# Performance work log

Measured on AMD Instinct MI355X. Metric: run time of the kernel, lower is better.

Reference implementation:

```python
import jax, jax.numpy as jnp
import numpy as np

N_HOST, N_FLOW = 20000, 200000
D_HOST, D_FLOW, D_H, D_OUT, L = 64, 128, 256, 2, 2
E = 2000000


def _mean_agg(x_src, src, dst, num_dst):
    # SAGEConv default 'mean' neighbor aggregation: mean of source features per destination node.
    msg = x_src[src]                                            # [E, D]
    s = jax.ops.segment_sum(msg, dst, num_segments=num_dst)     # [num_dst, D]
    cnt = jax.ops.segment_sum(jnp.ones((src.shape[0],), x_src.dtype), dst, num_segments=num_dst)
    return s / jnp.maximum(cnt, 1.0)[:, None]


def setup_inputs() -> dict:
    key = jax.random.key(0)
    ks = jax.random.split(key, 20)
    s = 0.02
    inp = {
        'x_host': jax.random.normal(ks[0], (N_HOST, D_HOST), jnp.float32),
        'x_flow': jax.random.normal(ks[1], (N_FLOW, D_FLOW), jnp.float32),
        'eidx_hf_src': jax.random.randint(ks[2], (E,), 0, N_HOST, jnp.int32),
        'eidx_hf_dst': jax.random.randint(ks[3], (E,), 0, N_FLOW, jnp.int32),
        'eidx_fh_src': jax.random.randint(ks[4], (E,), 0, N_FLOW, jnp.int32),
        'eidx_fh_dst': jax.random.randint(ks[5], (E,), 0, N_HOST, jnp.int32),
        'host_proj_W': jax.random.normal(ks[6], (D_HOST, D_H), jnp.float32) * s,
        'host_proj_b': jnp.zeros((D_H,), jnp.float32),
        'flow_proj_W': jax.random.normal(ks[7], (D_FLOW, D_H), jnp.float32) * s,
        'flow_proj_b': jnp.zeros((D_H,), jnp.float32),
        # per-layer SAGEConv params: lin_l (neighbor agg, with bias), lin_r (root, no bias)
        'Wl_hf': jax.random.normal(ks[8], (L, D_H, D_H), jnp.float32) * s,
        'bl_hf': jnp.zeros((L, D_H), jnp.float32),
        'Wr_hf': jax.random.normal(ks[9], (L, D_H, D_H), jnp.float32) * s,
        'Wl_fh': jax.random.normal(ks[10], (L, D_H, D_H), jnp.float32) * s,
        'bl_fh': jnp.zeros((L, D_H), jnp.float32),
        'Wr_fh': jax.random.normal(ks[11], (L, D_H, D_H), jnp.float32) * s,
        'lin_W': jax.random.normal(ks[12], (D_H, D_OUT), jnp.float32) * s,
        'lin_b': jnp.zeros((D_OUT,), jnp.float32),
    }
    return inp


def reference(x_host, x_flow, eidx_hf_src, eidx_hf_dst, eidx_fh_src, eidx_fh_dst,
              host_proj_W, host_proj_b, flow_proj_W, flow_proj_b,
              Wl_hf, bl_hf, Wr_hf, Wl_fh, bl_fh, Wr_fh, lin_W, lin_b):
    n_host, n_flow = x_host.shape[0], x_flow.shape[0]
    h = jax.nn.relu(x_host @ host_proj_W + host_proj_b)   # [n_host, D_H]
    f = jax.nn.relu(x_flow @ flow_proj_W + flow_proj_b)   # [n_flow, D_H]
    for i in range(Wl_hf.shape[0]):
        # host -> flow SAGEConv
        agg_f = _mean_agg(h, eidx_hf_src, eidx_hf_dst, n_flow)
        new_f = agg_f @ Wl_hf[i] + bl_hf[i] + f @ Wr_hf[i]
        # flow -> host SAGEConv
        agg_h = _mean_agg(f, eidx_fh_src, eidx_fh_dst, n_host)
        new_h = agg_h @ Wl_fh[i] + bl_fh[i] + h @ Wr_fh[i]
        h = jax.nn.leaky_relu(new_h, 0.01)
        f = jax.nn.leaky_relu(new_f, 0.01)
    return f @ lin_W + lin_b  # logits for flow nodes [n_flow, D_OUT]
```

## Files before the change

### kernel.cpp

```cpp
#include <hip/hip_runtime.h>

#define NH    20000
#define NF    200000
#define DHOST 64
#define DFLOW 128
#define DHID  256
#define NE    2000000

typedef __attribute__((ext_vector_type(8))) short s16x8;
typedef __attribute__((ext_vector_type(4))) float f32x4;

__device__ __forceinline__ unsigned short f2bf(float x) {
    unsigned u = __builtin_bit_cast(unsigned, x);
    unsigned r = (u + 0x7fffu + ((u >> 16) & 1u)) >> 16;
    return (unsigned short)r;
}
__device__ __forceinline__ float bf2f(unsigned short h) {
    unsigned u = ((unsigned)h) << 16;
    return __builtin_bit_cast(float, u);
}

typedef const __attribute__((address_space(1))) unsigned int guint;
typedef __attribute__((address_space(3))) unsigned int luint;
__device__ __forceinline__ void gld16(const void* g, void* l) {
    __builtin_amdgcn_global_load_lds((guint*)g, (luint*)l, 16, 0, 0);
}

__device__ __forceinline__ void dq8(uint2 u, float s, float* a) {
#pragma unroll
    for (int j = 0; j < 4; ++j) {
        a[j]     += s * (float)((signed char)(u.x >> (8 * j)));
        a[4 + j] += s * (float)((signed char)(u.y >> (8 * j)));
    }
}

__global__ void zero_k(int* __restrict__ p, int n) {
    int i = blockIdx.x * 256 + threadIdx.x;
    if (i < n) p[i] = 0;
}

__global__ __launch_bounds__(256) void tpose_k(const float* __restrict__ W, unsigned short* __restrict__ Wt, int K) {
    __shared__ float T[32][33];
    int bx = blockIdx.x, by = blockIdx.y;
    const float* Wz = W + (size_t)blockIdx.z * K * 256;
    unsigned short* Wtz = Wt + (size_t)blockIdx.z * K * 256;
    int tx = threadIdx.x & 31, ty = threadIdx.x >> 5;
#pragma unroll
    for (int i = 0; i < 4; ++i) {
        int k = by * 32 + ty + i * 8;
        T[ty + i * 8][tx] = Wz[(size_t)k * 256 + bx * 32 + tx];
    }
    __syncthreads();
#pragma unroll
    for (int i = 0; i < 4; ++i) {
        int n = bx * 32 + ty + i * 8;
        Wtz[(size_t)n * K + by * 32 + tx] = f2bf(T[tx][ty + i * 8]);
    }
}

__global__ void scan1_k(const int* __restrict__ in, int n, int* __restrict__ out, int* __restrict__ bsum) {
    __shared__ int wsum[4];
    int t = threadIdx.x;
    int lane = t & 63, wave = t >> 6;
    int idx = blockIdx.x * 1024 + t * 4;
    int v[4]; int s = 0;
#pragma unroll
    for (int i = 0; i < 4; ++i) { v[i] = (idx + i < n) ? in[idx + i] : 0; s += v[i]; }
    int inc = s;
#pragma unroll
    for (int off = 1; off < 64; off <<= 1) { int u = __shfl_up(inc, off); if (lane >= off) inc += u; }
    if (lane == 63) wsum[wave] = inc;
    __syncthreads();
    int woff = 0;
    for (int w = 0; w < wave; ++w) woff += wsum[w];
    int ex = woff + inc - s;
#pragma unroll
    for (int i = 0; i < 4; ++i) { if (idx + i < n) out[idx + i] = ex; ex += v[i]; }
    if (t == 255) bsum[blockIdx.x] = woff + inc;
}

__global__ __launch_bounds__(256) void histAB(const int* __restrict__ dstA, const int* __restrict__ dstB,
                                              int E, int* __restrict__ gbhA, int* __restrict__ gbhB) {
    __shared__ int lh[391];
    const int g = blockIdx.y;
    const int* dst = g ? dstB : dstA;
    int* gbh = g ? gbhB : gbhA;
    const int SH = g ? 6 : 9;
    const int NBKT = g ? 313 : 391;
    for (int b = threadIdx.x; b < NBKT; b += 256) lh[b] = 0;
    __syncthreads();
#pragma unroll
    for (int k = 0; k < 8; ++k) {
        int i = blockIdx.x * 2048 + k * 256 + threadIdx.x;
        if (i < E) atomicAdd(&lh[dst[i] >> SH], 1);
    }
    __syncthreads();
    for (int b = threadIdx.x; b < NBKT; b += 256) if (lh[b]) atomicAdd(&gbh[b], lh[b]);
}

__global__ void initcur_k(int* __restrict__ bko, int* __restrict__ gcur, int nbkt, int E) {
    int i = blockIdx.x * 256 + threadIdx.x;
    if (i < nbkt) gcur[i] = bko[i];
    if (i == nbkt) bko[nbkt] = E;
}

__global__ __launch_bounds__(256) void binpassAB(const int* __restrict__ srcA, const int* __restrict__ dstA,
                                                 const int* __restrict__ srcB, const int* __restrict__ dstB,
                                                 int E, int* __restrict__ gcurA, int* __restrict__ gcurB,
                                                 int* __restrict__ pairsA, int* __restrict__ pairsB) {
    __shared__ int lh[391], resv[391], lc[391];
    const int g = blockIdx.y;
    const int* src = g ? srcB : srcA;
    const int* dst = g ? dstB : dstA;
    int* gcur = g ? gcurB : gcurA;
    int* pairs = g ? pairsB : pairsA;
    const int SH = g ? 6 : 9;
    const int NBKT = g ? 313 : 391;
    const int MSK = (1 << SH) - 1;
    const int tid = threadIdx.x;
    const int e0 = blockIdx.x * 8192;
    for (int b = tid; b < NBKT; b += 256) { lh[b] = 0; lc[b] = 0; }
    __syncthreads();
#pragma unroll 4
    for (int k = 0; k < 32; ++k) {
        int i = e0 + k * 256 + tid;
        if (i < E) atomicAdd(&lh[dst[i] >> SH], 1);
    }
    __syncthreads();
    for (int b = tid; b < NBKT; b += 256) if (lh[b]) resv[b] = atomicAdd(&gcur[b], lh[b]);
    __syncthreads();
#pragma unroll 4
    for (int k = 0; k < 32; ++k) {
        int i = e0 + k * 256 + tid;
        if (i < E) {
            int d = dst[i];
            int b = d >> SH;
            int p = resv[b] + atomicAdd(&lc[b], 1);
            pairs[p] = src[i] | ((d & MSK) << 18);
        }
    }
}

__global__ __launch_bounds__(256) void csrfinAB(const int* __restrict__ pairsA, const int* __restrict__ bkoA,
                                                const int* __restrict__ pairsB, const int* __restrict__ bkoB,
                                                int NBA, int E,
                                                int* __restrict__ rpA, int* __restrict__ colA,
                                                int* __restrict__ rpB, int* __restrict__ colB) {
    __shared__ int cnt[512], pos[512];
    __shared__ int wsum[4];
    const int tid = threadIdx.x;
    const bool isA = (int)blockIdx.x < NBA;
    const int b = isA ? blockIdx.x : blockIdx.x - NBA;
    const int SH = isA ? 9 : 6;
    const int NPB = isA ? 512 : 64;
    const int N = isA ? NF : NH;
    const int* pairs = isA ? pairsA : pairsB;
    const int* bko = isA ? bkoA : bkoB;
    int* rowptr = isA ? rpA : rpB;
    int* col = isA ? colA : colB;
    const int nb = b << SH;
    const int beg = bko[b], end = bko[b + 1];
    for (int i = tid; i < NPB; i += 256) cnt[i] = 0;
    __syncthreads();
    for (int i = beg + tid; i < end; i += 256) atomicAdd(&cnt[pairs[i] >> 18], 1);
    __syncthreads();
    int lane = tid & 63, wave = tid >> 6;
    if (NPB == 512) {
        int a = cnt[2 * tid], b2 = cnt[2 * tid + 1];
        int s = a + b2, incl = s;
#pragma unroll
        for (int off = 1; off < 64; off <<= 1) { int u = __shfl_up(incl, off); if (lane >= off) incl += u; }
        if (lane == 63) wsum[wave] = incl;
        __syncthreads();
        int woff = 0;
        for (int w = 0; w < wave; ++w) woff += wsum[w];
        int ex = woff + incl - s;
        pos[2 * tid] = ex; pos[2 * tid + 1] = ex + a;
    } else {
        if (tid < NPB) {
            int a = cnt[tid], incl = a;
#pragma unroll
            for (int off = 1; off < 64; off <<= 1) { int u = __shfl_up(incl, off); if (lane >= off) incl += u; }
            pos[tid] = incl - a;
        }
    }
    __syncthreads();
    for (int i = tid; i < NPB; i += 256) {
        int node = nb + i;
        if (node < N) rowptr[node] = beg + pos[i];
    }
    if (tid == 0 && end == E) rowptr[N] = E;
    __syncthreads();
    for (int i = beg + tid; i < end; i += 256) {
        int pk = pairs[i];
        int p = atomicAdd(&pos[pk >> 18], 1);
        col[beg + p] = pk & 0x3FFFF;
    }
}

__global__ __launch_bounds__(256) void agg8_q8(const signed char* __restrict__ qf,
                                               const float* __restrict__ scl,
                                               const int* __restrict__ rowptr,
                                               const int* __restrict__ col,
                                               unsigned short* __restrict__ outp, int n) {
    int w = (blockIdx.x << 2) + (threadIdx.x >> 6);
    if (w >= n) return;
    int lane = threadIdx.x & 63;
    int half = lane >> 5, l5 = lane & 31;
    int beg = rowptr[w], end = rowptr[w + 1];
    int T = end - beg;
    const signed char* base = qf + l5 * 8;
    float a0[8], a1[8], a2[8], a3[8], a4[8], a5[8], a6[8], a7[8];
#pragma unroll
    for (int j = 0; j < 8; ++j) {
        a0[j] = 0.f; a1[j] = 0.f; a2[j] = 0.f; a3[j] = 0.f;
        a4[j] = 0.f; a5[j] = 0.f; a6[j] = 0.f; a7[j] = 0.f;
    }
    int i = beg;
    int nb16 = T >> 4;
    {
        const int* cp = col + beg + half * 8;
        for (int k = 0; k < nb16; ++k) {
            int c0 = cp[k * 16 + 0], c1 = cp[k * 16 + 1], c2 = cp[k * 16 + 2], c3 = cp[k * 16 + 3];
            int c4 = cp[k * 16 + 4], c5 = cp[k * 16 + 5], c6 = cp[k * 16 + 6], c7 = cp[k * 16 + 7];
            uint2 u0 = *reinterpret_cast<const uint2*>(base + (size_t)c0 * DHID);
            uint2 u1 = *reinterpret_cast<const uint2*>(base + (size_t)c1 * DHID);
            uint2 u2 = *reinterpret_cast<const uint2*>(base + (size_t)c2 * DHID);
            uint2 u3 = *reinterpret_cast<const uint2*>(base + (size_t)c3 * DHID);
            uint2 u4 = *reinterpret_cast<const uint2*>(base + (size_t)c4 * DHID);
            uint2 u5 = *reinterpret_cast<const uint2*>(base + (size_t)c5 * DHID);
            uint2 u6 = *reinterpret_cast<const uint2*>(base + (size_t)c6 * DHID);
            uint2 u7 = *reinterpret_cast<const uint2*>(base + (size_t)c7 * DHID);
            float s0 = scl[c0], s1 = scl[c1], s2 = scl[c2], s3 = scl[c3];
            float s4 = scl[c4], s5 = scl[c5], s6 = scl[c6], s7 = scl[c7];
            dq8(u0, s0, a0); dq8(u1, s1, a1); dq8(u2, s2, a2); dq8(u3, s3, a3);
            dq8(u4, s4, a4); dq8(u5, s5, a5); dq8(u6, s6, a6); dq8(u7, s7, a7);
        }
    }
    i += nb16 * 16;
    if (end - i >= 8) {
        const int* cp = col + i + half * 4;
        int c0 = cp[0], c1 = cp[1], c2 = cp[2], c3 = cp[3];
        uint2 u0 = *reinterpret_cast<const uint2*>(base + (size_t)c0 * DHID);
        uint2 u1 = *reinterpret_cast<const uint2*>(base + (size_t)c1 * DHID);
        uint2 u2 = *reinterpret_cast<const uint2*>(base + (size_t)c2 * DHID);
        uint2 u3 = *reinterpret_cast<const uint2*>(base + (size_t)c3 * DHID);
        float s0 = scl[c0], s1 = scl[c1], s2 = scl[c2], s3 = scl[c3];
        dq8(u0, s0, a0); dq8(u1, s1, a1); dq8(u2, s2, a2); dq8(u3, s3, a3);
        i += 8;
    }
    for (int e = i + half; e < end; e += 2) {
        int c = col[e];
        uint2 u = *reinterpret_cast<const uint2*>(base + (size_t)c * DHID);
        dq8(u, scl[c], a0);
    }
    int deg = T > 0 ? T : 1;
    float inv = 1.0f / (float)deg;
    s16x8 o;
#pragma unroll
    for (int j = 0; j < 8; ++j) {
        float s = ((a0[j] + a1[j]) + (a2[j] + a3[j])) + ((a4[j] + a5[j]) + (a6[j] + a7[j]));
        s += __shfl_xor(s, 32);
        o[j] = (short)f2bf(s * inv);
    }
    if (half == 0)
        *reinterpret_cast<s16x8*>(outp + (size_t)w * DHID + l5 * 8) = o;
}

__device__ __forceinline__ unsigned swz(unsigned r, unsigned cb) {
    return r * 128u + (cb ^ ((r & 7u) << 4));
}

union SmU {
    struct { char A[64 * 128]; char B[256 * 128]; } st;
    unsigned short tile[64][256];
};

__device__ __forceinline__ void pass64(const unsigned short* A, const unsigned short* Wt,
                                       int m0, int M, int lane, int wave, int wr, int wc,
                                       f32x4 (&acc)[2][4], SmU& sm) {
    for (int k0 = 0; k0 < DHID; k0 += 64) {
        __syncthreads();
        {
            int r = wave * 8 + (lane >> 3);
            int gr = m0 + r; if (gr >= M) gr = M - 1;
            int gs = (lane & 7) ^ (r & 7);
            gld16(A + (size_t)gr * DHID + k0 + gs * 8, sm.st.A + wave * 1024);
        }
#pragma unroll
        for (int i = 0; i < 4; ++i) {
            int u = wave * 4 + i;
            int nn = u * 8 + (lane >> 3);
            int gs = (lane & 7) ^ (nn & 7);
            gld16(Wt + (size_t)nn * DHID + k0 + gs * 8, sm.st.B + u * 1024);
        }
        __syncthreads();
#pragma unroll
        for (int kk = 0; kk < 2; ++kk) {
            s16x8 ar[2], br[4];
            unsigned colb = (unsigned)(kk * 64 + (lane >> 4) * 16);
#pragma unroll
            for (int mf = 0; mf < 2; ++mf)
                ar[mf] = *reinterpret_cast<const s16x8*>(sm.st.A + swz((unsigned)(wr * 32 + mf * 16 + (lane & 15)), colb));
#pragma unroll
            for (int nf = 0; nf < 4; ++nf)
                br[nf] = *reinterpret_cast<const s16x8*>(sm.st.B + swz((unsigned)(wc * 64 + nf * 16 + (lane & 15)), colb));
#pragma unroll
            for (int mf = 0; mf < 2; ++mf)
#pragma unroll
                for (int nf = 0; nf < 4; ++nf)
                    acc[mf][nf] = __builtin_amdgcn_mfma_f32_16x16x32_bf16(ar[mf], br[nf], acc[mf][nf], 0, 0, 0);
        }
    }
}

template<int ACT, int POST>
__device__ __forceinline__ void epi64(f32x4 (&acc)[2][4], const float* bias, SmU& sm,
                                      int m0, int M, int lane, int wave, int wr, int wc,
                                      unsigned short* outp, signed char* q, float* scl) {
    const int col0 = wc * 64 + (lane & 15);
    float bc[4];
#pragma unroll
    for (int nf = 0; nf < 4; ++nf) bc[nf] = bias[col0 + nf * 16];
    if (POST == 0) {
#pragma unroll
        for (int mf = 0; mf < 2; ++mf) {
            int row = m0 + wr * 32 + mf * 16 + (lane >> 4) * 4;
#pragma unroll
            for (int j = 0; j < 4; ++j) {
                if (row + j < M) {
#pragma unroll
                    for (int nf = 0; nf < 4; ++nf) {
                        float v = acc[mf][nf][j] + bc[nf];
                        if (ACT == 1) v = fmaxf(v, 0.0f);
                        else if (ACT == 2) v = v > 0.0f ? v : 0.01f * v;
                        outp[(size_t)(row + j) * DHID + col0 + nf * 16] = f2bf(v);
                    }
                }
            }
        }
        return;
    }
    __syncthreads();
#pragma unroll
    for (int mf = 0; mf < 2; ++mf) {
        int rl = wr * 32 + mf * 16 + (lane >> 4) * 4;
#pragma unroll
        for (int j = 0; j < 4; ++j)
#pragma unroll
            for (int nf = 0; nf < 4; ++nf) {
                float v = acc[mf][nf][j] + bc[nf];
                if (ACT == 1) v = fmaxf(v, 0.0f);
                else if (ACT == 2) v = v > 0.0f ? v : 0.01f * v;
                sm.tile[rl + j][col0 + nf * 16] = f2bf(v);
            }
    }
    __syncthreads();
    const int half = lane >> 5, l5 = lane & 31;
    for (int t = 0; t < 4; ++t) {
        int local = wave * 8 + half * 4 + t;
        int node = m0 + local;
        s16x8 tr = *reinterpret_cast<const s16x8*>(&sm.tile[local][l5 * 8]);
        float v[8]; float m = 0.0f;
#pragma unroll
        for (int j = 0; j < 8; ++j) { v[j] = bf2f((unsigned short)tr[j]); m = fmaxf(m, fabsf(v[j])); }
#pragma unroll
        for (int off = 1; off < 32; off <<= 1) m = fmaxf(m, __shfl_xor(m, off));
        if (node < M) {
            if (POST == 1)
                *reinterpret_cast<s16x8*>(outp + (size_t)node * DHID + l5 * 8) = tr;
            float si = (m > 0.0f) ? 127.0f / m : 0.0f;
            if (l5 == 0) scl[node] = m * (1.0f / 127.0f);
            uint2 pk;
            pk.x = ((unsigned)((int)__builtin_rintf(v[0] * si) & 255))
                 | ((unsigned)((int)__builtin_rintf(v[1] * si) & 255) << 8)
                 | ((unsigned)((int)__builtin_rintf(v[2] * si) & 255) << 16)
                 | ((unsigned)((int)__builtin_rintf(v[3] * si) & 255) << 24);
            pk.y = ((unsigned)((int)__builtin_rintf(v[4] * si) & 255))
                 | ((unsigned)((int)__builtin_rintf(v[5] * si) & 255) << 8)
                 | ((unsigned)((int)__builtin_rintf(v[6] * si) & 255) << 16)
                 | ((unsigned)((int)__builtin_rintf(v[7] * si) & 255) << 24);
            *reinterpret_cast<uint2*>(q + (size_t)node * DHID + l5 * 8) = pk;
        }
    }
}

template<int ACT, int FUSE, int POST>
__global__ __launch_bounds__(512) void mgemm64(const unsigned short* A1, const unsigned short* W1t,
                                               const float* __restrict__ bias,
                                               const unsigned short* A2, const unsigned short* W2t,
                                               unsigned short* outp, signed char* q, float* scl, int M) {
    __shared__ SmU sm;
    const int tid = threadIdx.x;
    const int lane = tid & 63, wave = tid >> 6;
    const int wr = wave >> 2, wc = wave & 3;
    const int m0 = blockIdx.x * 64;
    f32x4 acc[2][4];
#pragma unroll
    for (int a = 0; a < 2; ++a)
#pragma unroll
        for (int b = 0; b < 4; ++b) acc[a][b] = (f32x4)0.0f;
    pass64(A1, W1t, m0, M, lane, wave, wr, wc, acc, sm);
    if (FUSE) pass64(A2, W2t, m0, M, lane, wave, wr, wc, acc, sm);
    epi64<ACT, POST>(acc, bias, sm, m0, M, lane, wave, wr, wc, outp, q, scl);
}

template<int K1, int ACT, int POST>
__global__ __launch_bounds__(512) void mgemm64_f32(const float* __restrict__ A1, const unsigned short* W1t,
                                                   const float* __restrict__ bias,
                                                   unsigned short* outp, signed char* q, float* scl, int M) {
    __shared__ SmU sm;
    const int tid = threadIdx.x;
    const int lane = tid & 63, wave = tid >> 6;
    const int wr = wave >> 2, wc = wave & 3;
    const int m0 = blockIdx.x * 64;
    f32x4 acc[2][4];
#pragma unroll
    for (int a = 0; a < 2; ++a)
#pragma unroll
        for (int b = 0; b < 4; ++b) acc[a][b] = (f32x4)0.0f;

    for (int k0 = 0; k0 < K1; k0 += 64) {
        __syncthreads();
        {
            int r = tid >> 3, gc = tid & 7;
            int gr = m0 + r; if (gr >= M) gr = M - 1;
            const float* src = A1 + (size_t)gr * K1 + k0 + gc * 8;
            float4 v0 = *reinterpret_cast<const float4*>(src);
            float4 v1 = *reinterpret_cast<const float4*>(src + 4);
            s16x8 o;
            o[0] = (short)f2bf(v0.x); o[1] = (short)f2bf(v0.y);
            o[2] = (short)f2bf(v0.z); o[3] = (short)f2bf(v0.w);
            o[4] = (short)f2bf(v1.x); o[5] = (short)f2bf(v1.y);
            o[6] = (short)f2bf(v1.z); o[7] = (short)f2bf(v1.w);
            *reinterpret_cast<s16x8*>(sm.st.A + swz((unsigned)r, (unsigned)(gc * 16))) = o;
        }
#pragma unroll
        for (int i = 0; i < 4; ++i) {
            int u = wave * 4 + i;
            int nn = u * 8 + (lane >> 3);
            int gs = (lane & 7) ^ (nn & 7);
            gld16(W1t + (size_t)nn * K1 + k0 + gs * 8, sm.st.B + u * 1024);
        }
        __syncthreads();
#pragma unroll
        for (int kk = 0; kk < 2; ++kk) {
            s16x8 ar[2], br[4];
            unsigned colb = (unsigned)(kk * 64 + (lane >> 4) * 16);
#pragma unroll
            for (int mf = 0; mf < 2; ++mf)
                ar[mf] = *reinterpret_cast<const s16x8*>(sm.st.A + swz((unsigned)(wr * 32 + mf * 16 + (lane & 15)), colb));
#pragma unroll
            for (int nf = 0; nf < 4; ++nf)
                br[nf] = *reinterpret_cast<const s16x8*>(sm.st.B + swz((unsigned)(wc * 64 + nf * 16 + (lane & 15)), colb));
#pragma unroll
            for (int mf = 0; mf < 2; ++mf)
#pragma unroll
                for (int nf = 0; nf < 4; ++nf)
                    acc[mf][nf] = __builtin_amdgcn_mfma_f32_16x16x32_bf16(ar[mf], br[nf], acc[mf][nf], 0, 0, 0);
        }
    }
    epi64<ACT, POST>(acc, bias, sm, m0, M, lane, wave, wr, wc, outp, q, scl);
}

template<int HEAD>
__global__ __launch_bounds__(512) void mgemm_faq(const unsigned short* Fin, const unsigned short* Wrt,
                                                 const float* __restrict__ bias,
                                                 const signed char* __restrict__ Hq,
                                                 const float* __restrict__ sclH,
                                                 const int* __restrict__ rowptr,
                                                 const int* __restrict__ colv,
                                                 unsigned short* Fout,
                                                 const float* __restrict__ linW,
                                                 const float* __restrict__ linb,
                                                 float* __restrict__ outHead, int M) {
    __shared__ SmU sm;
    const int tid = threadIdx.x;
    const int lane = tid & 63, wave = tid >> 6;
    const int wr = wave >> 2, wc = wave & 3;
    const int m0 = blockIdx.x * 64;
    f32x4 acc[2][4];
#pragma unroll
    for (int a = 0; a < 2; ++a)
#pragma unroll
        for (int b = 0; b < 4; ++b) acc[a][b] = (f32x4)0.0f;

    pass64(Fin, Wrt, m0, M, lane, wave, wr, wc, acc, sm);
    __syncthreads();

    const int col0 = wc * 64 + (lane & 15);
    float bc[4];
#pragma unroll
    for (int nf = 0; nf < 4; ++nf) bc[nf] = bias[col0 + nf * 16];
#pragma unroll
    for (int mf = 0; mf < 2; ++mf) {
        int rl = wr * 32 + mf * 16 + (lane >> 4) * 4;
#pragma unroll
        for (int j = 0; j < 4; ++j)
#pragma unroll
            for (int nf = 0; nf < 4; ++nf)
                sm.tile[rl + j][col0 + nf * 16] = f2bf(acc[mf][nf][j] + bc[nf]);
    }
    __syncthreads();

    const int half = lane >> 5, l5 = lane & 31;
    const signed char* base = Hq + l5 * 8;
    float w0[8], w1[8], hb0 = 0.0f, hb1 = 0.0f;
    if (HEAD) {
#pragma unroll
        for (int j = 0; j < 8; ++j) {
            w0[j] = linW[(l5 * 8 + j) * 2 + 0];
            w1[j] = linW[(l5 * 8 + j) * 2 + 1];
        }
        hb0 = linb[0]; hb1 = linb[1];
    }
    for (int t = 0; t < 8; ++t) {
        int local = wave * 8 + t;
        int node = m0 + local;
        if (node >= M) break;
        int beg = rowptr[node], end = rowptr[node + 1];
        int T = end - beg;
        int nb8 = T >> 3;
        float a0[8], a1[8], a2[8], a3[8];
#pragma unroll
        for (int j = 0; j < 8; ++j) { a0[j] = 0.f; a1[j] = 0.f; a2[j] = 0.f; a3[j] = 0.f; }
        const int* cp = colv + beg + half * 4;
        for (int k = 0; k < nb8; ++k) {
            int c0 = cp[k * 8 + 0], c1 = cp[k * 8 + 1], c2 = cp[k * 8 + 2], c3 = cp[k * 8 + 3];
            uint2 u0 = *reinterpret_cast<const uint2*>(base + (size_t)c0 * DHID);
            uint2 u1 = *reinterpret_cast<const uint2*>(base + (size_t)c1 * DHID);
            uint2 u2 = *reinterpret_cast<const uint2*>(base + (size_t)c2 * DHID);
            uint2 u3 = *reinterpret_cast<const uint2*>(base + (size_t)c3 * DHID);
            float s0 = sclH[c0], s1 = sclH[c1], s2 = sclH[c2], s3 = sclH[c3];
            dq8(u0, s0, a0); dq8(u1, s1, a1); dq8(u2, s2, a2); dq8(u3, s3, a3);
        }
        for (int i = beg + nb8 * 8 + half; i < end; i += 2) {
            int c = colv[i];
            uint2 u = *reinterpret_cast<const uint2*>(base + (size_t)c * DHID);
            dq8(u, sclH[c], a0);
        }
        float inv = 1.0f / (float)(T > 0 ? T : 1);
        s16x8 tr = *reinterpret_cast<const s16x8*>(&sm.tile[local][l5 * 8]);
        float v[8];
        s16x8 o;
#pragma unroll
        for (int j = 0; j < 8; ++j) {
            float s = (a0[j] + a1[j]) + (a2[j] + a3[j]);
            s += __shfl_xor(s, 32);
            float x = bf2f((unsigned short)tr[j]) + s * inv;
            x = x > 0.0f ? x : 0.01f * x;
            v[j] = x; o[j] = (short)f2bf(x);
        }
        if (HEAD) {
            float p0 = 0.0f, p1 = 0.0f;
#pragma unroll
            for (int j = 0; j < 8; ++j) { p0 += v[j] * w0[j]; p1 += v[j] * w1[j]; }
#pragma unroll
            for (int off = 1; off < 32; off <<= 1) {
                p0 += __shfl_xor(p0, off);
                p1 += __shfl_xor(p1, off);
            }
            if (lane == 0) {
                outHead[(size_t)node * 2 + 0] = p0 + hb0;
                outHead[(size_t)node * 2 + 1] = p1 + hb1;
            }
        } else {
            if (half == 0)
                *reinterpret_cast<s16x8*>(Fout + (size_t)node * DHID + l5 * 8) = o;
        }
    }
}

extern "C" void kernel_launch(void* const* d_in, const int* in_sizes, int n_in,
                              void* d_out, int out_size, void* d_ws, size_t ws_size,
                              hipStream_t stream) {
    const float* x_host  = (const float*)d_in[0];
    const float* x_flow  = (const float*)d_in[1];
    const int*   hf_src  = (const int*)d_in[2];
    const int*   hf_dst  = (const int*)d_in[3];
    const int*   fh_src  = (const int*)d_in[4];
    const int*   fh_dst  = (const int*)d_in[5];
    const float* host_W  = (const float*)d_in[6];
    const float* host_b  = (const float*)d_in[7];
    const float* flow_W  = (const float*)d_in[8];
    const float* flow_b  = (const float*)d_in[9];
    const float* Wl_hf   = (const float*)d_in[10];
    const float* bl_hf   = (const float*)d_in[11];
    const float* Wr_hf   = (const float*)d_in[12];
    const float* Wl_fh   = (const float*)d_in[13];
    const float* bl_fh   = (const float*)d_in[14];
    const float* Wr_fh   = (const float*)d_in[15];
    const float* lin_W   = (const float*)d_in[16];
    const float* lin_b   = (const float*)d_in[17];

    char* ws = (char*)d_ws;
    size_t off = 0;
    auto alloc = [&](size_t bytes) -> char* {
        char* p = ws + off;
        off += (bytes + 255) & ~(size_t)255;
        return p;
    };
    typedef unsigned short u16;
    u16* F     = (u16*)alloc((size_t)NF * DHID * 2);
    u16* H     = (u16*)alloc((size_t)NH * DHID * 2);
    u16* AggH  = (u16*)alloc((size_t)NH * DHID * 2);
    signed char* Fq = (signed char*)alloc((size_t)NF * DHID);
    signed char* Hq = (signed char*)alloc((size_t)NH * DHID);
    float* sclF = (float*)alloc((size_t)NF * 4);
    float* sclH = (float*)alloc((size_t)NH * 4);
    u16* hostWt = (u16*)alloc((size_t)DHID * DHOST * 2);
    u16* flowWt = (u16*)alloc((size_t)DHID * DFLOW * 2);
    u16* WlhfT  = (u16*)alloc((size_t)2 * DHID * DHID * 2);
    u16* WrhfT  = (u16*)alloc((size_t)2 * DHID * DHID * 2);
    u16* WlfhT  = (u16*)alloc((size_t)2 * DHID * DHID * 2);
    u16* WrfhT  = (u16*)alloc((size_t)2 * DHID * DHID * 2);
    float* zbias = (float*)alloc(DHID * 4);
    int* rp_hf  = (int*)alloc((size_t)(NF + 1) * 4);
    int* col_hf = (int*)alloc((size_t)NE * 4);
    int* rp_fh  = (int*)alloc((size_t)(NH + 1) * 4);
    int* col_fh = (int*)alloc((size_t)NE * 4);
    int* pairsA = (int*)alloc((size_t)NE * 4);
    int* pairsB = (int*)alloc((size_t)NE * 4);
    int* gbh2   = (int*)alloc(1024 * 4);
    int* bkoA   = (int*)alloc(513 * 4);
    int* bkoB   = (int*)alloc(513 * 4);
    int* gcurA  = (int*)alloc(512 * 4);
    int* gcurB  = (int*)alloc(512 * 4);
    int* junk   = (int*)alloc(4);
    int* gbhA = gbh2, *gbhB = gbh2 + 512;

    const int NBKT_HF = (NF + 511) / 512;
    const int NBKT_FH = (NH + 63) / 64;

    zero_k<<<4, 256, 0, stream>>>(gbh2, 1024);
    histAB<<<dim3((NE + 2047) / 2048, 2), 256, 0, stream>>>(hf_dst, fh_dst, NE, gbhA, gbhB);
    scan1_k<<<1, 256, 0, stream>>>(gbhA, NBKT_HF, bkoA, junk);
    scan1_k<<<1, 256, 0, stream>>>(gbhB, NBKT_FH, bkoB, junk);
    initcur_k<<<2, 256, 0, stream>>>(bkoA, gcurA, NBKT_HF, NE);
    initcur_k<<<2, 256, 0, stream>>>(bkoB, gcurB, NBKT_FH, NE);
    binpassAB<<<dim3((NE + 8191) / 8192, 2), 256, 0, stream>>>(hf_src, hf_dst, fh_src, fh_dst, NE,
                                                               gcurA, gcurB, pairsA, pairsB);
    csrfinAB<<<NBKT_HF + NBKT_FH, 256, 0, stream>>>(pairsA, bkoA, pairsB, bkoB, NBKT_HF, NE,
                                                    rp_hf, col_hf, rp_fh, col_fh);

    zero_k<<<1, 256, 0, stream>>>((int*)zbias, DHID);
    tpose_k<<<dim3(8, DHOST / 32, 1), 256, 0, stream>>>(host_W, hostWt, DHOST);
    tpose_k<<<dim3(8, DFLOW / 32, 1), 256, 0, stream>>>(flow_W, flowWt, DFLOW);
    tpose_k<<<dim3(8, 8, 2), 256, 0, stream>>>(Wl_hf, WlhfT, DHID);
    tpose_k<<<dim3(8, 8, 2), 256, 0, stream>>>(Wr_hf, WrhfT, DHID);
    tpose_k<<<dim3(8, 8, 2), 256, 0, stream>>>(Wl_fh, WlfhT, DHID);
    tpose_k<<<dim3(8, 8, 2), 256, 0, stream>>>(Wr_fh, WrfhT, DHID);

    mgemm64_f32<DHOST, 1, 0><<<(NH + 63) / 64, 512, 0, stream>>>(x_host, hostWt, host_b, H, nullptr, nullptr, NH);
    mgemm64_f32<DFLOW, 1, 1><<<(NF + 63) / 64, 512, 0, stream>>>(x_flow, flowWt, flow_b, F, Fq, sclF, NF);

    {
        const u16* wl_hf = WlhfT;
        const u16* wr_hf = WrhfT;
        const u16* wl_fh = WlfhT;
        const u16* wr_fh = WrfhT;

        mgemm64<0, 0, 2><<<(NH + 63) / 64, 512, 0, stream>>>(H, wl_hf, zbias, H, wl_hf,
                                                             nullptr, Hq, sclH, NH);
        agg8_q8<<<(NH + 3) / 4, 256, 0, stream>>>(Fq, sclF, rp_fh, col_fh, AggH, NH);
        mgemm_faq<0><<<(NF + 63) / 64, 512, 0, stream>>>(F, wr_hf, bl_hf, Hq, sclH,
                                                         rp_hf, col_hf, F,
                                                         nullptr, nullptr, nullptr, NF);
        mgemm64<2, 1, 0><<<(NH + 63) / 64, 512, 0, stream>>>(AggH, wl_fh, bl_fh, H, wr_fh,
                                                             H, nullptr, nullptr, NH);
    }

    {
        const u16* wl_hf = WlhfT + (size_t)DHID * DHID;
        const u16* wr_hf = WrhfT + (size_t)DHID * DHID;
        const float* b_hf = bl_hf + DHID;

        mgemm64<0, 0, 2><<<(NH + 63) / 64, 512, 0, stream>>>(H, wl_hf, zbias, H, wl_hf,
                                                             nullptr, Hq, sclH, NH);
        mgemm_faq<1><<<(NF + 63) / 64, 512, 0, stream>>>(F, wr_hf, b_hf, Hq, sclH,
                                                         rp_hf, col_hf, nullptr,
                                                         lin_W, lin_b, (float*)d_out, NF);
    }
}
```

Before: 736.4 us.

## Fuse host aggregation with flow SAGE GEMM into one interleaved launch

Turns the layer-0 flow GEMM+aggregation body and the host mean-aggregation into device functions and merges them into one kernel. Within each group of 9 blocks, 5 blocks do flow GEMM tiles and 4 blocks do host aggregation with 8 waves each. The goal is to overlap the latency-bound gather with the MFMA-heavy GEMM and to remove one launch and its serialization. In exchange, aggregation blocks now carry the GEMM's large shared-memory allocation and 512-thread shape, which may reduce how many of them are resident at once.

```diff
diff --git a/kernel.cpp b/kernel.cpp
--- a/kernel.cpp
+++ b/kernel.cpp
@@ -198,14 +198,11 @@
     }
 }
 
-__global__ __launch_bounds__(256) void agg8_q8(const signed char* __restrict__ qf,
-                                               const float* __restrict__ scl,
-                                               const int* __restrict__ rowptr,
-                                               const int* __restrict__ col,
-                                               unsigned short* __restrict__ outp, int n) {
-    int w = (blockIdx.x << 2) + (threadIdx.x >> 6);
-    if (w >= n) return;
-    int lane = threadIdx.x & 63;
+__device__ __forceinline__ void agg_node(int w, const signed char* __restrict__ qf,
+                                         const float* __restrict__ scl,
+                                         const int* __restrict__ rowptr,
+                                         const int* __restrict__ col,
+                                         unsigned short* __restrict__ outp, int lane) {
     int half = lane >> 5, l5 = lane & 31;
     int beg = rowptr[w], end = rowptr[w + 1];
     int T = end - beg;
@@ -464,21 +461,20 @@
 }
 
 template<int HEAD>
-__global__ __launch_bounds__(512) void mgemm_faq(const unsigned short* Fin, const unsigned short* Wrt,
-                                                 const float* __restrict__ bias,
-                                                 const signed char* __restrict__ Hq,
-                                                 const float* __restrict__ sclH,
-                                                 const int* __restrict__ rowptr,
-                                                 const int* __restrict__ colv,
-                                                 unsigned short* Fout,
-                                                 const float* __restrict__ linW,
-                                                 const float* __restrict__ linb,
-                                                 float* __restrict__ outHead, int M) {
-    __shared__ SmU sm;
-    const int tid = threadIdx.x;
-    const int lane = tid & 63, wave = tid >> 6;
+__device__ __forceinline__ void faq_body(int fb,
+                                         const unsigned short* Fin, const unsigned short* Wrt,
+                                         const float* __restrict__ bias,
+                                         const signed char* __restrict__ Hq,
+                                         const float* __restrict__ sclH,
+                                         const int* __restrict__ rowptr,
+                                         const int* __restrict__ colv,
+                                         unsigned short* Fout,
+                                         const float* __restrict__ linW,
+                                         const float* __restrict__ linb,
+                                         float* __restrict__ outHead, int M,
+                                         SmU& sm, int lane, int wave) {
     const int wr = wave >> 2, wc = wave & 3;
-    const int m0 = blockIdx.x * 64;
+    const int m0 = fb * 64;
     f32x4 acc[2][4];
 #pragma unroll
     for (int a = 0; a < 2; ++a)
@@ -568,6 +564,46 @@
             if (half == 0)
                 *reinterpret_cast<s16x8*>(Fout + (size_t)node * DHID + l5 * 8) = o;
         }
+    }
+}
+
+__global__ __launch_bounds__(512) void mgemm_fah(const unsigned short* Fin, const unsigned short* Wrt,
+                                                 const float* __restrict__ bias,
+                                                 const signed char* __restrict__ Hq,
+                                                 const float* __restrict__ sclH,
+                                                 const int* __restrict__ rowptr,
+                                                 const int* __restrict__ colv,
+                                                 const float* __restrict__ linW,
+                                                 const float* __restrict__ linb,
+                                                 float* __restrict__ outHead, int M) {
+    __shared__ SmU sm;
+    faq_body<1>(blockIdx.x, Fin, Wrt, bias, Hq, sclH, rowptr, colv, nullptr,
+                linW, linb, outHead, M, sm, threadIdx.x & 63, threadIdx.x >> 6);
+}
+
+__global__ __launch_bounds__(512) void faq_agg_k(const unsigned short* Fin, const unsigned short* Wrt,
+                                                 const float* __restrict__ bias,
+                                                 const signed char* __restrict__ Hq,
+                                                 const float* __restrict__ sclH,
+                                                 const int* __restrict__ rp_hf,
+                                                 const int* __restrict__ col_hf,
+                                                 unsigned short* Fout,
+                                                 const signed char* __restrict__ Fq,
+                                                 const float* __restrict__ sclF,
+                                                 const int* __restrict__ rp_fh,
+                                                 const int* __restrict__ col_fh,
+                                                 unsigned short* __restrict__ AggH, int MF) {
+    __shared__ SmU sm;
+    const int lane = threadIdx.x & 63, wave = threadIdx.x >> 6;
+    const int grpb = blockIdx.x / 9, rem = blockIdx.x % 9;
+    if (rem < 5) {
+        int fb = grpb * 5 + rem;
+        faq_body<0>(fb, Fin, Wrt, bias, Hq, sclH, rp_hf, col_hf, Fout,
+                    nullptr, nullptr, nullptr, MF, sm, lane, wave);
+    } else {
+        int w = (grpb * 4 + (rem - 5)) * 8 + wave;
+        if (w < NH)
+            agg_node(w, Fq, sclF, rp_fh, col_fh, AggH, lane);
     }
 }
 
@@ -662,10 +698,8 @@
 
         mgemm64<0, 0, 2><<<(NH + 63) / 64, 512, 0, stream>>>(H, wl_hf, zbias, H, wl_hf,
                                                              nullptr, Hq, sclH, NH);
-        agg8_q8<<<(NH + 3) / 4, 256, 0, stream>>>(Fq, sclF, rp_fh, col_fh, AggH, NH);
-        mgemm_faq<0><<<(NF + 63) / 64, 512, 0, stream>>>(F, wr_hf, bl_hf, Hq, sclH,
-                                                         rp_hf, col_hf, F,
-                                                         nullptr, nullptr, nullptr, NF);
+        faq_agg_k<<<9 * 625, 512, 0, stream>>>(F, wr_hf, bl_hf, Hq, sclH, rp_hf, col_hf, F,
+                                               Fq, sclF, rp_fh, col_fh, AggH, NF);
         mgemm64<2, 1, 0><<<(NH + 63) / 64, 512, 0, stream>>>(AggH, wl_fh, bl_fh, H, wr_fh,
                                                              H, nullptr, nullptr, NH);
     }
@@ -677,8 +711,8 @@
 
         mgemm64<0, 0, 2><<<(NH + 63) / 64, 512, 0, stream>>>(H, wl_hf, zbias, H, wl_hf,
                                                              nullptr, Hq, sclH, NH);
-        mgemm_faq<1><<<(NF + 63) / 64, 512, 0, stream>>>(F, wr_hf, b_hf, Hq, sclH,
-                                                         rp_hf, col_hf, nullptr,
-                                                         lin_W, lin_b, (float*)d_out, NF);
-    }
-}
+        mgemm_fah<<<(NF + 63) / 64, 512, 0, stream>>>(F, wr_hf, b_hf, Hq, sclH,
+                                                      rp_hf, col_hf, lin_W, lin_b,
+                                                      (float*)d_out, NF);
+    }
+}
```

New measurement: 892.4 us. 1.21x slower.
